# Optimization experiments

Measured on AMD Instinct MI355X. Metric: run time of the kernel, lower is better.

The kernel has to match this reference:

```python
import jax, jax.numpy as jnp
import numpy as np

N = 100000
E = 3200000
F_IN = 512
HID = 16
NUM_CLASSES = 2
NUM_GRAPHS = 256


def setup_inputs() -> dict:
    key = jax.random.key(0)
    k = jax.random.split(key, 8)
    x = jax.random.normal(k[0], (N, F_IN), dtype=jnp.float32)
    edge_index = jax.random.randint(k[1], (2, E), 0, N, dtype=jnp.int64)
    batch = jnp.sort(jax.random.randint(k[2], (N,), 0, NUM_GRAPHS, dtype=jnp.int64))
    # Glorot init like PyG GCNConv, biases zero-init
    W1 = jax.random.normal(k[3], (F_IN, HID), dtype=jnp.float32) * (2.0 / (F_IN + HID)) ** 0.5
    b1 = jnp.zeros((HID,), dtype=jnp.float32)
    W2 = jax.random.normal(k[4], (HID, NUM_CLASSES), dtype=jnp.float32) * (2.0 / (HID + NUM_CLASSES)) ** 0.5
    b2 = jnp.zeros((NUM_CLASSES,), dtype=jnp.float32)
    return {"x": x, "W1": W1, "b1": b1, "W2": W2, "b2": b2,
            "edge_index": edge_index, "batch": batch}


def _gcn_conv(x, W, b, src, dst, n):
    # PyG GCNConv: linear first, add self loops, symmetric deg^-1/2 normalization,
    # scatter-add messages from src to dst, then bias.
    h = x @ W                                        # [N, out]
    loops = jnp.arange(n, dtype=src.dtype)
    s = jnp.concatenate([src, loops])                # [E+N]
    d = jnp.concatenate([dst, loops])                # [E+N]
    deg = jax.ops.segment_sum(jnp.ones_like(d, dtype=h.dtype), d, num_segments=n)
    dinv = jax.lax.rsqrt(deg)                        # deg >= 1 due to self loops
    norm = dinv[s] * dinv[d]                         # [E+N]
    out = jax.ops.segment_sum(norm[:, None] * h[s], d, num_segments=n)
    return out + b


def reference(x, W1, b1, W2, b2, edge_index, batch):
    src, dst = edge_index[0], edge_index[1]
    h = jax.nn.relu(_gcn_conv(x, W1, b1, src, dst, N))
    h = _gcn_conv(h, W2, b2, src, dst, N)
    # global_mean_pool over graph ids
    sums = jax.ops.segment_sum(h, batch, num_segments=NUM_GRAPHS)
    counts = jax.ops.segment_sum(jnp.ones((N,), dtype=h.dtype), batch, num_segments=NUM_GRAPHS)
    pooled = sums / jnp.maximum(counts, 1.0)[:, None]  # [G, num_classes]
    return jax.nn.log_softmax(pooled, axis=1)
```

## Files before the change

### kernel.cpp

```cpp
#include <hip/hip_runtime.h>
#include <hip/hip_fp16.h>

#define N_NODES 100000
#define N_EDGES 3200000
#define F_INN 512
#define NGR 256
#define BSH 6
#define NBIN 1563
#define KBB 256
#define CHUNK (N_EDGES / KBB)
#define CAP 2560

typedef __attribute__((ext_vector_type(8))) short bf16x8;
typedef __attribute__((ext_vector_type(4))) float f32x4;

__device__ __forceinline__ uint f2bf2(float a, float b) {
  uint ua = __float_as_uint(a), ub = __float_as_uint(b);
  uint ra = (ua + 0x7FFF + ((ua >> 16) & 1)) >> 16;
  uint rb = (ub + 0x7FFF + ((ub >> 16) & 1)) >> 16;
  return ra | (rb << 16);
}

__global__ __launch_bounds__(512) void k_bin(const int* __restrict__ ei,
                                             int* __restrict__ bincur,
                                             int* __restrict__ rec,
                                             const float* __restrict__ W,
                                             ushort* __restrict__ Wt) {
  if (blockIdx.x == KBB) {
    for (int tid = threadIdx.x; tid < 16 * 512; tid += 512) {
      int n = tid >> 9;
      int k = tid & 511;
      uint u = __float_as_uint(W[k * 16 + n]);
      Wt[tid] = (ushort)((u + 0x7FFF + ((u >> 16) & 1)) >> 16);
    }
    return;
  }
  __shared__ int h[NBIN];
  __shared__ int base[NBIN];
  for (int t = threadIdx.x; t < NBIN; t += 512) h[t] = 0;
  __syncthreads();
  int e0 = blockIdx.x * CHUNK;
  for (int i = threadIdx.x; i < CHUNK; i += 512)
    atomicAdd(&h[ei[N_EDGES + e0 + i] >> BSH], 1);
  __syncthreads();
  for (int t = threadIdx.x; t < NBIN; t += 512) {
    int c = h[t];
    base[t] = t * CAP + (c ? atomicAdd(&bincur[t], c) : 0);
    h[t] = 0;
  }
  __syncthreads();
  for (int i = threadIdx.x; i < CHUNK; i += 512) {
    int s = ei[e0 + i];
    int d = ei[N_EDGES + e0 + i];
    int k = d >> BSH;
    int pos = base[k] + atomicAdd(&h[k], 1);
    rec[pos] = (s << BSH) | (d & 63);
  }
}

__global__ __launch_bounds__(256) void k_gemm1(const float* __restrict__ X,
                                               const ushort* __restrict__ Wt,
                                               const int* __restrict__ rec,
                                               const int* __restrict__ bincur,
                                               __half* __restrict__ T1h) {
  __shared__ int hh[64];
  const int t = threadIdx.x;
  if (t < 64) hh[t] = 0;
  __syncthreads();
  {
    int cnt = bincur[blockIdx.x];
    const int* rb = rec + (size_t)blockIdx.x * CAP;
    for (int i = t; i < cnt; i += 256) atomicAdd(&hh[rb[i] & 63], 1);
  }

  const int lane = t & 63;
  const int w = t >> 6;
  const int c16 = lane & 15;
  const int g = lane >> 4;
  const int arow = blockIdx.x * 64 + w * 16 + c16;
  const bool rv = arow < N_NODES;
  const float* xrow = X + (size_t)arow * F_INN + g * 8;
  const ushort* brow = Wt + c16 * 512 + g * 8;

  f32x4 acc = {0.f, 0.f, 0.f, 0.f};
#pragma unroll
  for (int ks = 0; ks < 16; ++ks) {
    float4 v0 = rv ? *(const float4*)(xrow + ks * 32)     : make_float4(0.f, 0.f, 0.f, 0.f);
    float4 v1 = rv ? *(const float4*)(xrow + ks * 32 + 4) : make_float4(0.f, 0.f, 0.f, 0.f);
    uint au[4] = { f2bf2(v0.x, v0.y), f2bf2(v0.z, v0.w),
                   f2bf2(v1.x, v1.y), f2bf2(v1.z, v1.w) };
    bf16x8 a = *(const bf16x8*)au;
    bf16x8 b = *(const bf16x8*)(brow + ks * 32);
    acc = __builtin_amdgcn_mfma_f32_16x16x32_bf16(a, b, acc, 0, 0, 0);
  }

  __syncthreads();
  int lbase = w * 16 + g * 4;
  int rbase = blockIdx.x * 64 + lbase;
#pragma unroll
  for (int j = 0; j < 4; ++j) {
    int r = rbase + j;
    if (r < N_NODES) {
      float di = rsqrtf((float)hh[lbase + j] + 1.0f);
      T1h[(size_t)r * 16 + c16] = __float2half(di * acc[j]);
    }
  }
}

__global__ __launch_bounds__(256) void k_agg1(const int* __restrict__ rec,
                                              const int* __restrict__ bincur,
                                              const __half* __restrict__ T1h,
                                              const float* __restrict__ b1,
                                              const float* __restrict__ W2,
                                              float* __restrict__ T2) {
  __shared__ int recs[CAP];
  __shared__ int recs2[CAP];
  __shared__ float accs[64 * 17];
  __shared__ int hh[64], excl[64], cur[64];
  int k = blockIdx.x, t = threadIdx.x;
  int n0 = k << BSH;
  int cnt = bincur[k];
  if (t < 64) hh[t] = 0;
  __syncthreads();
  for (int i = t; i < cnt; i += 256) {
    int v = rec[(size_t)k * CAP + i];
    recs[i] = v;
    atomicAdd(&hh[v & 63], 1);
  }
  int node = n0 + (t >> 2);
  int q = t & 3;
  bool nv = node < N_NODES;
  float a0 = 0.f, a1 = 0.f, a2 = 0.f, a3 = 0.f;
  if (nv) {
    uint2 u = *(const uint2*)(T1h + (size_t)node * 16 + q * 4);
    float2 f0 = __half22float2(*reinterpret_cast<__half2*>(&u.x));
    float2 f1 = __half22float2(*reinterpret_cast<__half2*>(&u.y));
    a0 = f0.x; a1 = f0.y; a2 = f1.x; a3 = f1.y;
  }
  __syncthreads();
  if (t < 64) {
    int c = hh[t];
    int sc = c;
#pragma unroll
    for (int o = 1; o < 64; o <<= 1) {
      int u = __shfl_up(sc, o);
      if (t >= o) sc += u;
    }
    excl[t] = sc - c;
    cur[t] = 0;
  }
  __syncthreads();
  for (int i = t; i < cnt; i += 256) {
    int v = recs[i];
    int dl = v & 63;
    int pos = excl[dl] + atomicAdd(&cur[dl], 1);
    recs2[pos] = v >> BSH;
  }
  __syncthreads();
  int myc = hh[t >> 2];
  int r = excl[t >> 2];
  int e = r + myc;
  for (; r + 1 < e; r += 2) {
    int s0 = recs2[r], s1 = recs2[r + 1];
    uint2 ua = *(const uint2*)(T1h + (size_t)s0 * 16 + q * 4);
    uint2 ub = *(const uint2*)(T1h + (size_t)s1 * 16 + q * 4);
    float2 fa0 = __half22float2(*reinterpret_cast<__half2*>(&ua.x));
    float2 fa1 = __half22float2(*reinterpret_cast<__half2*>(&ua.y));
    float2 fb0 = __half22float2(*reinterpret_cast<__half2*>(&ub.x));
    float2 fb1 = __half22float2(*reinterpret_cast<__half2*>(&ub.y));
    a0 += fa0.x + fb0.x; a1 += fa0.y + fb0.y;
    a2 += fa1.x + fb1.x; a3 += fa1.y + fb1.y;
  }
  if (r < e) {
    int s = recs2[r];
    uint2 u = *(const uint2*)(T1h + (size_t)s * 16 + q * 4);
    float2 f0 = __half22float2(*reinterpret_cast<__half2*>(&u.x));
    float2 f1 = __half22float2(*reinterpret_cast<__half2*>(&u.y));
    a0 += f0.x; a1 += f0.y; a2 += f1.x; a3 += f1.y;
  }
  float dd = nv ? rsqrtf((float)myc + 1.0f) : 0.f;
  float* rowp = &accs[(t >> 2) * 17 + q * 4];
  rowp[0] = dd * a0; rowp[1] = dd * a1; rowp[2] = dd * a2; rowp[3] = dd * a3;
  __syncthreads();
  if (t < 64) {
    int n = n0 + t;
    if (n < N_NODES) {
      float dd2 = rsqrtf((float)hh[t] + 1.0f);
      float s0 = 0.f, s1 = 0.f;
#pragma unroll
      for (int c = 0; c < 16; ++c) {
        float hv = fmaxf(accs[t * 17 + c] + b1[c], 0.f);
        s0 = fmaf(hv, W2[c * 2 + 0], s0);
        s1 = fmaf(hv, W2[c * 2 + 1], s1);
      }
      T2[(size_t)n * 2 + 0] = dd2 * s0;
      T2[(size_t)n * 2 + 1] = dd2 * s1;
    }
  }
}

__global__ __launch_bounds__(256) void k_agg2(const int* __restrict__ rec,
                                              const int* __restrict__ bincur,
                                              const float* __restrict__ T2,
                                              const int* __restrict__ batch,
                                              float* __restrict__ pool,
                                              float* __restrict__ gcnt) {
  __shared__ int recs[CAP];
  __shared__ int recs2[CAP];
  __shared__ float sm[128];
  __shared__ int hh[64], excl[64], cur[64];
  int k = blockIdx.x, t = threadIdx.x;
  int n0 = k << BSH;
  int cnt = bincur[k];
  if (t < 64) hh[t] = 0;
  __syncthreads();
  for (int i = t; i < cnt; i += 256) {
    int v = rec[(size_t)k * CAP + i];
    recs[i] = v;
    atomicAdd(&hh[v & 63], 1);
  }
  __syncthreads();
  if (t < 64) {
    int c = hh[t];
    int sc = c;
#pragma unroll
    for (int o = 1; o < 64; o <<= 1) {
      int u = __shfl_up(sc, o);
      if (t >= o) sc += u;
    }
    excl[t] = sc - c;
    cur[t] = 0;
  }
  __syncthreads();
  for (int i = t; i < cnt; i += 256) {
    int v = recs[i];
    int dl = v & 63;
    int pos = excl[dl] + atomicAdd(&cur[dl], 1);
    recs2[pos] = v >> BSH;
  }
  __syncthreads();
  if (t < 128) {
    int nl = t >> 1, c = t & 1;
    int n = n0 + nl;
    bool nv = n < N_NODES;
    float acc = nv ? T2[(size_t)n * 2 + c] : 0.f;
    int r = excl[nl], e = r + hh[nl];
    for (; r + 1 < e; r += 2) {
      int s0 = recs2[r], s1 = recs2[r + 1];
      acc += T2[(size_t)s0 * 2 + c] + T2[(size_t)s1 * 2 + c];
    }
    if (r < e) acc += T2[(size_t)recs2[r] * 2 + c];
    sm[t] = nv ? rsqrtf((float)hh[nl] + 1.0f) * acc : 0.f;
  }
  __syncthreads();
  if (t < 64) {
    int n = n0 + t;
    bool valid = n < N_NODES;
    int b = valid ? batch[n] : -1;
    float vx = sm[2 * t], vy = sm[2 * t + 1];
    int b0 = __shfl(b, 0);
    if (__all(b == b0)) {
      if (b0 >= 0) {
#pragma unroll
        for (int o = 32; o > 0; o >>= 1) {
          vx += __shfl_xor(vx, o);
          vy += __shfl_xor(vy, o);
        }
        if (t == 0) {
          atomicAdd(&pool[b0 * 2 + 0], vx);
          atomicAdd(&pool[b0 * 2 + 1], vy);
          atomicAdd(&gcnt[b0], 64.0f);
        }
      }
    } else if (valid) {
      atomicAdd(&pool[b * 2 + 0], vx);
      atomicAdd(&pool[b * 2 + 1], vy);
      atomicAdd(&gcnt[b], 1.0f);
    }
  }
}

__global__ __launch_bounds__(256) void k_final(const float* __restrict__ pool,
                                               const float* __restrict__ gcnt,
                                               const float* __restrict__ b2,
                                               float* __restrict__ out) {
  int g = threadIdx.x;
  if (g < NGR) {
    float c = fmaxf(gcnt[g], 1.0f);
    float p0 = pool[g * 2 + 0] / c + b2[0];
    float p1 = pool[g * 2 + 1] / c + b2[1];
    float m = fmaxf(p0, p1);
    float l = logf(expf(p0 - m) + expf(p1 - m));
    out[g * 2 + 0] = p0 - m - l;
    out[g * 2 + 1] = p1 - m - l;
  }
}

extern "C" void kernel_launch(void* const* d_in, const int* in_sizes, int n_in,
                              void* d_out, int out_size, void* d_ws, size_t ws_size,
                              hipStream_t stream) {
  const float* x  = (const float*)d_in[0];
  const float* W1 = (const float*)d_in[1];
  const float* b1 = (const float*)d_in[2];
  const float* W2 = (const float*)d_in[3];
  const float* b2 = (const float*)d_in[4];
  const int*   ei = (const int*)d_in[5];
  const int*   bt = (const int*)d_in[6];
  float* out = (float*)d_out;

  char* ws = (char*)d_ws;
  int*   bincur = (int*)ws;    ws += (size_t)NBIN * 4;
  float* pool   = (float*)ws;  ws += 2 * NGR * 4;
  float* gcnt   = (float*)ws;  ws += NGR * 4;
  ushort* wt    = (ushort*)ws; ws += (size_t)16 * 512 * 2;
  int*   rec    = (int*)ws;    ws += (size_t)NBIN * CAP * 4;
  __half* t1h   = (__half*)ws; ws += (size_t)N_NODES * 16 * 2;
  float* t2     = (float*)ws;  ws += (size_t)N_NODES * 2 * 4;

  hipMemsetAsync(bincur, 0, (size_t)(NBIN + 3 * NGR) * 4, stream);

  k_bin   <<<KBB + 1, 512, 0, stream>>>(ei, bincur, rec, W1, wt);
  k_gemm1 <<<NBIN, 256, 0, stream>>>(x, wt, rec, bincur, t1h);
  k_agg1  <<<NBIN, 256, 0, stream>>>(rec, bincur, t1h, b1, W2, t2);
  k_agg2  <<<NBIN, 256, 0, stream>>>(rec, bincur, t2, bt, pool, gcnt);
  k_final <<<1, 256, 0, stream>>>(pool, gcnt, b2, out);
}
```

Baseline: 195.1 us.

## Fuse final log-softmax into agg2 via last-block ticket, cache dst indices, unroll gathers

The final pooling/log-softmax kernel is folded into k_agg2: each block takes a ticket after a threadfence, and the last block reads pool/gcnt atomically and writes the output, removing one kernel launch. k_bin keeps destination indices in registers between the histogram and scatter passes instead of reloading them from global memory. The gather loops in both aggregation kernels are unrolled to four edges per iteration for more memory-level parallelism. The costs are a global atomic per block, register pressure from the 25-entry array, and reliance on fence ordering for correctness.

```diff
diff --git a/kernel.cpp b/kernel.cpp
--- a/kernel.cpp
+++ b/kernel.cpp
@@ -9,6 +9,7 @@
 #define NBIN 1563
 #define KBB 256
 #define CHUNK (N_EDGES / KBB)
+#define EPT 25
 #define CAP 2560
 
 typedef __attribute__((ext_vector_type(8))) short bf16x8;
@@ -19,6 +20,14 @@
   uint ra = (ua + 0x7FFF + ((ua >> 16) & 1)) >> 16;
   uint rb = (ub + 0x7FFF + ((ub >> 16) & 1)) >> 16;
   return ra | (rb << 16);
+}
+
+__device__ __forceinline__ void acc_h8(const __half* base, int s, int q,
+                                       float& a0, float& a1, float& a2, float& a3) {
+  uint2 u = *(const uint2*)(base + (size_t)s * 16 + q * 4);
+  float2 f0 = __half22float2(*reinterpret_cast<__half2*>(&u.x));
+  float2 f1 = __half22float2(*reinterpret_cast<__half2*>(&u.y));
+  a0 += f0.x; a1 += f0.y; a2 += f1.x; a3 += f1.y;
 }
 
 __global__ __launch_bounds__(512) void k_bin(const int* __restrict__ ei,
@@ -40,8 +49,13 @@
   for (int t = threadIdx.x; t < NBIN; t += 512) h[t] = 0;
   __syncthreads();
   int e0 = blockIdx.x * CHUNK;
-  for (int i = threadIdx.x; i < CHUNK; i += 512)
-    atomicAdd(&h[ei[N_EDGES + e0 + i] >> BSH], 1);
+  int dreg[EPT];
+  int nj = 0;
+  for (int i = threadIdx.x; i < CHUNK; i += 512, ++nj) {
+    int d = ei[N_EDGES + e0 + i];
+    dreg[nj] = d;
+    atomicAdd(&h[d >> BSH], 1);
+  }
   __syncthreads();
   for (int t = threadIdx.x; t < NBIN; t += 512) {
     int c = h[t];
@@ -49,9 +63,10 @@
     h[t] = 0;
   }
   __syncthreads();
-  for (int i = threadIdx.x; i < CHUNK; i += 512) {
+  nj = 0;
+  for (int i = threadIdx.x; i < CHUNK; i += 512, ++nj) {
     int s = ei[e0 + i];
-    int d = ei[N_EDGES + e0 + i];
+    int d = dreg[nj];
     int k = d >> BSH;
     int pos = base[k] + atomicAdd(&h[k], 1);
     rec[pos] = (s << BSH) | (d & 63);
@@ -131,12 +146,7 @@
   int q = t & 3;
   bool nv = node < N_NODES;
   float a0 = 0.f, a1 = 0.f, a2 = 0.f, a3 = 0.f;
-  if (nv) {
-    uint2 u = *(const uint2*)(T1h + (size_t)node * 16 + q * 4);
-    float2 f0 = __half22float2(*reinterpret_cast<__half2*>(&u.x));
-    float2 f1 = __half22float2(*reinterpret_cast<__half2*>(&u.y));
-    a0 = f0.x; a1 = f0.y; a2 = f1.x; a3 = f1.y;
-  }
+  if (nv) acc_h8(T1h, node, q, a0, a1, a2, a3);
   __syncthreads();
   if (t < 64) {
     int c = hh[t];
@@ -160,24 +170,14 @@
   int myc = hh[t >> 2];
   int r = excl[t >> 2];
   int e = r + myc;
-  for (; r + 1 < e; r += 2) {
-    int s0 = recs2[r], s1 = recs2[r + 1];
-    uint2 ua = *(const uint2*)(T1h + (size_t)s0 * 16 + q * 4);
-    uint2 ub = *(const uint2*)(T1h + (size_t)s1 * 16 + q * 4);
-    float2 fa0 = __half22float2(*reinterpret_cast<__half2*>(&ua.x));
-    float2 fa1 = __half22float2(*reinterpret_cast<__half2*>(&ua.y));
-    float2 fb0 = __half22float2(*reinterpret_cast<__half2*>(&ub.x));
-    float2 fb1 = __half22float2(*reinterpret_cast<__half2*>(&ub.y));
-    a0 += fa0.x + fb0.x; a1 += fa0.y + fb0.y;
-    a2 += fa1.x + fb1.x; a3 += fa1.y + fb1.y;
-  }
-  if (r < e) {
-    int s = recs2[r];
-    uint2 u = *(const uint2*)(T1h + (size_t)s * 16 + q * 4);
-    float2 f0 = __half22float2(*reinterpret_cast<__half2*>(&u.x));
-    float2 f1 = __half22float2(*reinterpret_cast<__half2*>(&u.y));
-    a0 += f0.x; a1 += f0.y; a2 += f1.x; a3 += f1.y;
-  }
+  for (; r + 3 < e; r += 4) {
+    int s0 = recs2[r], s1 = recs2[r + 1], s2 = recs2[r + 2], s3 = recs2[r + 3];
+    acc_h8(T1h, s0, q, a0, a1, a2, a3);
+    acc_h8(T1h, s1, q, a0, a1, a2, a3);
+    acc_h8(T1h, s2, q, a0, a1, a2, a3);
+    acc_h8(T1h, s3, q, a0, a1, a2, a3);
+  }
+  for (; r < e; ++r) acc_h8(T1h, recs2[r], q, a0, a1, a2, a3);
   float dd = nv ? rsqrtf((float)myc + 1.0f) : 0.f;
   float* rowp = &accs[(t >> 2) * 17 + q * 4];
   rowp[0] = dd * a0; rowp[1] = dd * a1; rowp[2] = dd * a2; rowp[3] = dd * a3;
@@ -203,12 +203,16 @@
                                               const int* __restrict__ bincur,
                                               const float* __restrict__ T2,
                                               const int* __restrict__ batch,
+                                              const float* __restrict__ b2,
                                               float* __restrict__ pool,
-                                              float* __restrict__ gcnt) {
+                                              float* __restrict__ gcnt,
+                                              int* __restrict__ ticket,
+                                              float* __restrict__ out) {
   __shared__ int recs[CAP];
   __shared__ int recs2[CAP];
   __shared__ float sm[128];
   __shared__ int hh[64], excl[64], cur[64];
+  __shared__ int isLast;
   int k = blockIdx.x, t = threadIdx.x;
   int n0 = k << BSH;
   int cnt = bincur[k];
@@ -245,11 +249,12 @@
     bool nv = n < N_NODES;
     float acc = nv ? T2[(size_t)n * 2 + c] : 0.f;
     int r = excl[nl], e = r + hh[nl];
-    for (; r + 1 < e; r += 2) {
-      int s0 = recs2[r], s1 = recs2[r + 1];
-      acc += T2[(size_t)s0 * 2 + c] + T2[(size_t)s1 * 2 + c];
-    }
-    if (r < e) acc += T2[(size_t)recs2[r] * 2 + c];
+    for (; r + 3 < e; r += 4) {
+      int s0 = recs2[r], s1 = recs2[r + 1], s2 = recs2[r + 2], s3 = recs2[r + 3];
+      acc += T2[(size_t)s0 * 2 + c] + T2[(size_t)s1 * 2 + c]
+           + T2[(size_t)s2 * 2 + c] + T2[(size_t)s3 * 2 + c];
+    }
+    for (; r < e; ++r) acc += T2[(size_t)recs2[r] * 2 + c];
     sm[t] = nv ? rsqrtf((float)hh[nl] + 1.0f) * acc : 0.f;
   }
   __syncthreads();
@@ -278,21 +283,20 @@
       atomicAdd(&gcnt[b], 1.0f);
     }
   }
-}
-
-__global__ __launch_bounds__(256) void k_final(const float* __restrict__ pool,
-                                               const float* __restrict__ gcnt,
-                                               const float* __restrict__ b2,
-                                               float* __restrict__ out) {
-  int g = threadIdx.x;
-  if (g < NGR) {
-    float c = fmaxf(gcnt[g], 1.0f);
-    float p0 = pool[g * 2 + 0] / c + b2[0];
-    float p1 = pool[g * 2 + 1] / c + b2[1];
+  if (t == 0) {
+    __threadfence();
+    int v = atomicAdd(ticket, 1);
+    isLast = (v == NBIN - 1);
+  }
+  __syncthreads();
+  if (isLast && t < NGR) {
+    float c = fmaxf(atomicAdd(&gcnt[t], 0.f), 1.0f);
+    float p0 = atomicAdd(&pool[t * 2 + 0], 0.f) / c + b2[0];
+    float p1 = atomicAdd(&pool[t * 2 + 1], 0.f) / c + b2[1];
     float m = fmaxf(p0, p1);
     float l = logf(expf(p0 - m) + expf(p1 - m));
-    out[g * 2 + 0] = p0 - m - l;
-    out[g * 2 + 1] = p1 - m - l;
+    out[t * 2 + 0] = p0 - m - l;
+    out[t * 2 + 1] = p1 - m - l;
   }
 }
 
@@ -312,16 +316,16 @@
   int*   bincur = (int*)ws;    ws += (size_t)NBIN * 4;
   float* pool   = (float*)ws;  ws += 2 * NGR * 4;
   float* gcnt   = (float*)ws;  ws += NGR * 4;
+  int*   ticket = (int*)ws;    ws += 4 * 4;
   ushort* wt    = (ushort*)ws; ws += (size_t)16 * 512 * 2;
   int*   rec    = (int*)ws;    ws += (size_t)NBIN * CAP * 4;
   __half* t1h   = (__half*)ws; ws += (size_t)N_NODES * 16 * 2;
   float* t2     = (float*)ws;  ws += (size_t)N_NODES * 2 * 4;
 
-  hipMemsetAsync(bincur, 0, (size_t)(NBIN + 3 * NGR) * 4, stream);
+  hipMemsetAsync(bincur, 0, (size_t)(NBIN + 3 * NGR + 4) * 4, stream);
 
   k_bin   <<<KBB + 1, 512, 0, stream>>>(ei, bincur, rec, W1, wt);
   k_gemm1 <<<NBIN, 256, 0, stream>>>(x, wt, rec, bincur, t1h);
   k_agg1  <<<NBIN, 256, 0, stream>>>(rec, bincur, t1h, b1, W2, t2);
-  k_agg2  <<<NBIN, 256, 0, stream>>>(rec, bincur, t2, bt, pool, gcnt);
-  k_final <<<1, 256, 0, stream>>>(pool, gcnt, b2, out);
-}
+  k_agg2  <<<NBIN, 256, 0, stream>>>(rec, bincur, t2, bt, b2, pool, gcnt, ticket, out);
+}
```

Measured after the change: 210.6 us. +7.9%, slower.
